# Kernel optimization log

Measured on AMD Instinct MI355X. Metric: run time of the kernel, lower is better.

The kernel has to match this reference:

```python
import jax, jax.numpy as jnp
import numpy as np


def _conv(x, w, b, pad):
    # x: (B,C,H,W), w: (O,I,kh,kw), NCHW conv with given padding
    y = jax.lax.conv_general_dilated(x, w, window_strides=(1, 1), padding=pad,
                                     dimension_numbers=('NCHW', 'OIHW', 'NCHW'))
    return y + b[None, :, None, None]


def _frn(x, eps):
    # FilterResponseNorm: normalize by rms over spatial dims (2,3)
    nu2 = jnp.mean(x * x, axis=(2, 3), keepdims=True)
    return x * jax.lax.rsqrt(nu2 + jnp.abs(eps))


def _mish(x):
    return x * jnp.tanh(jax.nn.softplus(x))


def setup_inputs() -> dict:
    key = jax.random.key(0)
    ks = jax.random.split(key, 9)
    B, C, H, W = 4, 256, 64, 64
    C16 = C // 16
    x = jax.random.normal(ks[0], (B, C, H, W), dtype=jnp.float32)
    s = 0.05
    wq = jax.random.normal(ks[1], (C16, C, 1, 3), dtype=jnp.float32) * s
    bq = jax.random.normal(ks[2], (C16,), dtype=jnp.float32) * s
    wk = jax.random.normal(ks[3], (C16, C, 3, 1), dtype=jnp.float32) * s
    bk = jax.random.normal(ks[4], (C16,), dtype=jnp.float32) * s
    wv = jax.random.normal(ks[5], (C, C, 1, 1), dtype=jnp.float32) * s
    bv = jax.random.normal(ks[6], (C,), dtype=jnp.float32) * s
    gamma = jax.random.normal(ks[7], (1,), dtype=jnp.float32) * 0.1
    eps_q = jnp.full((1, C16, 1, 1), 1e-6, dtype=jnp.float32)
    eps_k = jnp.full((1, C16, 1, 1), 1e-6, dtype=jnp.float32)
    return {"x": x, "wq": wq, "bq": bq, "wk": wk, "bk": bk,
            "wv": wv, "bv": bv, "gamma": gamma, "eps_q": eps_q, "eps_k": eps_k}


def reference(x, wq, bq, wk, bk, wv, bv, gamma, eps_q, eps_k):
    B, C, H, W = x.shape
    N = H * W
    # query branch: Conv2d(k=(1,3), pad=(0,1)) -> FRN -> Mish
    q = _mish(_frn(_conv(x, wq, bq, [(0, 0), (1, 1)]), eps_q))  # (B,C16,H,W)
    # key branch: Conv2d(k=(3,1), pad=(1,0)) -> FRN -> Mish
    k = _mish(_frn(_conv(x, wk, bk, [(1, 1), (0, 0)]), eps_k))  # (B,C16,H,W)
    q = q.reshape(B, -1, N)  # (B,C16,N)
    k = k.reshape(B, -1, N)  # (B,C16,N)
    # affinity[b,n,m] = sum_c q[b,c,n] * k[b,c,m]; softmax over m
    affinity = jnp.einsum('bcn,bcm->bnm', q, k)
    affinity = jax.nn.softmax(affinity, axis=-1)  # (B,N,N)
    v = _conv(x, wv, bv, [(0, 0), (0, 0)]).reshape(B, C, N)  # (B,C,N)
    # weights = v @ affinity^T : weights[b,c,j] = sum_n v[b,c,n] * affinity[b,j,n]
    weights = jnp.einsum('bcn,bjn->bcj', v, affinity).reshape(B, C, H, W)
    return gamma * weights + x
```

## Files before the change

### kernel.cpp

```cpp
#include <hip/hip_runtime.h>
#include <stdint.h>

#define NB 4
#define CC 256
#define C16 16
#define HH 64
#define WW 64
#define NN 4096

typedef __attribute__((ext_vector_type(8))) short short8;
typedef __attribute__((ext_vector_type(4))) float floatx4;
typedef __attribute__((ext_vector_type(16))) float floatx16;

#if __has_builtin(__builtin_amdgcn_exp2f)
#define EXP2(x) __builtin_amdgcn_exp2f(x)
#else
#define EXP2(x) exp2f(x)
#endif

__device__ __forceinline__ unsigned short f2bf(float f) {
    union { float f; unsigned u; } v; v.f = f;
    unsigned r = v.u + 0x7fffu + ((v.u >> 16) & 1u);
    return (unsigned short)(r >> 16);
}
__device__ __forceinline__ float bf2f(unsigned short h) {
    union { unsigned u; float f; } v; v.u = (unsigned)h << 16;
    return v.f;
}


__global__ __launch_bounds__(256) void prep_kernel(
        const float* __restrict__ x, const float* __restrict__ wv,
        const float* __restrict__ wq, const float* __restrict__ wk,
        unsigned short* __restrict__ xT, unsigned short* __restrict__ wvb,
        unsigned short* __restrict__ wqkb, float* __restrict__ nu2) {
    int bid = blockIdx.x;
    if (bid < 1024) {
        __shared__ float tile_t[64][65];
        int nt = bid & 63, ct = (bid >> 6) & 3, b = bid >> 8;
        int n0 = nt * 64, c0 = ct * 64;
        int tid = threadIdx.x;
        int rg = tid >> 4, f = tid & 15;
        const float* xb = x + ((size_t)b * CC + c0) * NN + n0;
#pragma unroll
        for (int p = 0; p < 4; ++p) {
            int c = p * 16 + rg;
            float4 v = *(const float4*)(xb + (size_t)c * NN + f * 4);
            tile_t[f * 4 + 0][c] = v.x;
            tile_t[f * 4 + 1][c] = v.y;
            tile_t[f * 4 + 2][c] = v.z;
            tile_t[f * 4 + 3][c] = v.w;
        }
        __syncthreads();
        unsigned short* xtb = xT + ((size_t)b * NN + n0) * CC + c0;
#pragma unroll
        for (int p = 0; p < 4; ++p) {
            int n = p * 16 + rg;
            ushort4 st;
            st.x = f2bf(tile_t[n][f * 4 + 0]);
            st.y = f2bf(tile_t[n][f * 4 + 1]);
            st.z = f2bf(tile_t[n][f * 4 + 2]);
            st.w = f2bf(tile_t[n][f * 4 + 3]);
            *(ushort4*)(xtb + (size_t)n * CC + f * 4) = st;
        }
    } else {
        int idx = (bid - 1024) * 256 + threadIdx.x;
        if (bid == 1024 && threadIdx.x < 128) nu2[threadIdx.x] = 0.f;
        if (idx < 16384) {
            float4 v = *(const float4*)(wv + idx * 4);
            ushort4 o;
            o.x = f2bf(v.x); o.y = f2bf(v.y); o.z = f2bf(v.z); o.w = f2bf(v.w);
            *(ushort4*)(wvb + idx * 4) = o;
        } else if (idx < 16384 + 6144) {
            int base = (idx - 16384) * 4;
#pragma unroll
            for (int u = 0; u < 4; ++u) {
                int e = base + u;
                int t = e / 12288;
                int i = e - t * 12288;
                int tap = i >> 12, o = (i >> 8) & 15, c = i & 255;
                const float* src = t ? wk : wq;
                wqkb[e] = f2bf(src[o * 768 + c * 3 + tap]);
            }
        }
    }
}

__global__ __launch_bounds__(256) void conv_kernel(
        const unsigned short* __restrict__ xT, const unsigned short* __restrict__ wvb,
        const unsigned short* __restrict__ wqkb, const float* __restrict__ bv,
        const float* __restrict__ bq, const float* __restrict__ bk,
        unsigned short* __restrict__ vb, unsigned short* __restrict__ qrawh,
        unsigned short* __restrict__ krawh, float* __restrict__ nu2) {
    int bid = blockIdx.x;
    int tid = threadIdx.x;
    int wv_ = tid >> 6, lane = tid & 63;
    int q16 = lane >> 4, c16 = lane & 15;
    if (bid < 512) {
        int ntile = bid & 63, b = (bid >> 6) & 3, ch = bid >> 8;
        int n0 = ntile * 64;
        int cb = ch * 128 + wv_ * 32;
        floatx4 fzero = {0.f, 0.f, 0.f, 0.f};
        floatx4 acc[2][4];
        for (int ct = 0; ct < 2; ++ct)
            for (int nt = 0; nt < 4; ++nt) acc[ct][nt] = fzero;
        const unsigned short* xb = xT + ((size_t)b * NN + n0) * CC;
        for (int kc = 0; kc < 8; ++kc) {
            int ko = kc * 32 + q16 * 8;
            short8 a0 = *(const short8*)(wvb + (size_t)(cb + c16) * CC + ko);
            short8 a1 = *(const short8*)(wvb + (size_t)(cb + 16 + c16) * CC + ko);
            short8 bf[4];
#pragma unroll
            for (int nt = 0; nt < 4; ++nt)
                bf[nt] = *(const short8*)(xb + (size_t)(nt * 16 + c16) * CC + ko);
#pragma unroll
            for (int nt = 0; nt < 4; ++nt) {
                acc[0][nt] = __builtin_amdgcn_mfma_f32_16x16x32_bf16(bf[nt], a0, acc[0][nt], 0, 0, 0);
                acc[1][nt] = __builtin_amdgcn_mfma_f32_16x16x32_bf16(bf[nt], a1, acc[1][nt], 0, 0, 0);
            }
        }
        float bv0 = bv[cb + c16], bv1 = bv[cb + 16 + c16];
        int off = 32 * 8 * (q16 >> 1) + (q16 & 1) * 4 + c16 * 8;
#pragma unroll
        for (int ct = 0; ct < 2; ++ct) {
            float bvv = ct ? bv1 : bv0;
#pragma unroll
            for (int nt = 0; nt < 4; ++nt) {
                size_t fb = (((size_t)b * 8 + ch * 4 + wv_) * 256 + (n0 >> 4) + nt) * 512;
                ushort4 st;
                st.x = f2bf(acc[ct][nt][0] + bvv);
                st.y = f2bf(acc[ct][nt][1] + bvv);
                st.z = f2bf(acc[ct][nt][2] + bvv);
                st.w = f2bf(acc[ct][nt][3] + bvv);
                *(ushort4*)(vb + fb + off + ct * 16 * 8) = st;
            }
        }
    } else {
        int cv = bid - 512;
        int nb2 = cv & 63, b = cv >> 6;
        int nl = nb2 * 64 + wv_ * 16 + c16;
        int h = nl >> 6, w = nl & 63;
        bool vm1 = (w != 0), vp1 = (w != 63);
        bool vm64 = (h != 0), vp64 = (h != 63);
        short8 zero8 = {0, 0, 0, 0, 0, 0, 0, 0};
        floatx4 accq = {0.f, 0.f, 0.f, 0.f}, acck = {0.f, 0.f, 0.f, 0.f};
        const unsigned short* xb = xT + (size_t)b * NN * CC;
        const unsigned short* wrow = wqkb + c16 * 256;
        for (int kc = 0; kc < 8; ++kc) {
            int ko = kc * 32 + q16 * 8;
            short8 b0 = *(const short8*)(xb + (size_t)nl * CC + ko);
            short8 bm1 = vm1 ? *(const short8*)(xb + (size_t)(nl - 1) * CC + ko) : zero8;
            short8 bp1 = vp1 ? *(const short8*)(xb + (size_t)(nl + 1) * CC + ko) : zero8;
            short8 bm64 = vm64 ? *(const short8*)(xb + (size_t)(nl - 64) * CC + ko) : zero8;
            short8 bp64 = vp64 ? *(const short8*)(xb + (size_t)(nl + 64) * CC + ko) : zero8;
            short8 aq0 = *(const short8*)(wrow + 0 * 4096 + ko);
            short8 aq1 = *(const short8*)(wrow + 1 * 4096 + ko);
            short8 aq2 = *(const short8*)(wrow + 2 * 4096 + ko);
            short8 ak0 = *(const short8*)(wrow + 12288 + 0 * 4096 + ko);
            short8 ak1 = *(const short8*)(wrow + 12288 + 1 * 4096 + ko);
            short8 ak2 = *(const short8*)(wrow + 12288 + 2 * 4096 + ko);
            accq = __builtin_amdgcn_mfma_f32_16x16x32_bf16(bm1, aq0, accq, 0, 0, 0);
            accq = __builtin_amdgcn_mfma_f32_16x16x32_bf16(b0, aq1, accq, 0, 0, 0);
            accq = __builtin_amdgcn_mfma_f32_16x16x32_bf16(bp1, aq2, accq, 0, 0, 0);
            acck = __builtin_amdgcn_mfma_f32_16x16x32_bf16(bm64, ak0, acck, 0, 0, 0);
            acck = __builtin_amdgcn_mfma_f32_16x16x32_bf16(b0, ak1, acck, 0, 0, 0);
            acck = __builtin_amdgcn_mfma_f32_16x16x32_bf16(bp64, ak2, acck, 0, 0, 0);
        }
        int nst = nb2 * 64 + wv_ * 16 + q16 * 4;
        float bqv = bq[c16], bkv = bk[c16];
        ushort4 sq4, sk4;
        float ssq = 0.f, ssk = 0.f;
        {
            float vq0 = accq[0] + bqv, vq1 = accq[1] + bqv, vq2 = accq[2] + bqv, vq3 = accq[3] + bqv;
            float vk0 = acck[0] + bkv, vk1 = acck[1] + bkv, vk2 = acck[2] + bkv, vk3 = acck[3] + bkv;
            sq4.x = f2bf(vq0); sq4.y = f2bf(vq1); sq4.z = f2bf(vq2); sq4.w = f2bf(vq3);
            sk4.x = f2bf(vk0); sk4.y = f2bf(vk1); sk4.z = f2bf(vk2); sk4.w = f2bf(vk3);
            ssq = vq0 * vq0 + vq1 * vq1 + vq2 * vq2 + vq3 * vq3;
            ssk = vk0 * vk0 + vk1 * vk1 + vk2 * vk2 + vk3 * vk3;
        }
        *(ushort4*)(qrawh + (size_t)(b * C16 + c16) * NN + nst) = sq4;
        *(ushort4*)(krawh + (size_t)(b * C16 + c16) * NN + nst) = sk4;
        ssq += __shfl_xor(ssq, 16, 64);
        ssq += __shfl_xor(ssq, 32, 64);
        ssk += __shfl_xor(ssk, 16, 64);
        ssk += __shfl_xor(ssk, 32, 64);
        if (lane < 16) {
            atomicAdd(nu2 + b * C16 + lane, ssq);
            atomicAdd(nu2 + 64 + b * C16 + lane, ssk);
        }
    }
}

__global__ __launch_bounds__(256) void frn_mish_kernel(
        const unsigned short* __restrict__ qrawh, const unsigned short* __restrict__ krawh,
        const float* __restrict__ nu2, const float* __restrict__ eps_q,
        const float* __restrict__ eps_k, unsigned short* __restrict__ qb,
        unsigned short* __restrict__ kb) {
    int blk = blockIdx.x;
    int tensor = blk >> 8;
    int b = (blk >> 6) & 3;
    int nch = blk & 63;
    const unsigned short* raw = tensor ? krawh : qrawh;
    const float* eps = tensor ? eps_k : eps_q;
    unsigned short* outp = tensor ? kb : qb;
    const float* nu = nu2 + tensor * 64 + b * C16;
    float scale = tensor ? 1.0f : 1.44269504f;
    int n = nch * 64 + (threadIdx.x & 63);
    int oq = threadIdx.x >> 6;
    ushort4 pk4;
#pragma unroll
    for (int i = 0; i < 4; ++i) {
        int o = oq * 4 + i;
        float r = bf2f(raw[(size_t)(b * C16 + o) * NN + n]);
        float v = r * rsqrtf(nu[o] * (1.f / (float)NN) + fabsf(eps[o]));
        float t = EXP2(v * 1.44269504f);
        float num = t * t + 2.0f * t;
        float m = (v * num) * __builtin_amdgcn_rcpf(num + 2.0f);
        if (v > 30.f) m = v;
        m *= scale;
        ((unsigned short*)&pk4)[i] = f2bf(m);
    }
    size_t base = ((size_t)b * 128 + (n >> 5)) * 512 + (size_t)(n & 31) * 8
                + (size_t)(oq >> 1) * 256 + (oq & 1) * 4;
    *(ushort4*)(outp + base) = pk4;
}

__device__ __forceinline__ void pack_half(
        const floatx16& sc, int h, short8* A, float* lsum) {
    unsigned pk[4];
    float ls = 0.f;
#pragma unroll
    for (int p = 0; p < 4; ++p) {
        float e0 = EXP2(sc[8 * h + 2 * p]);
        float e1 = EXP2(sc[8 * h + 2 * p + 1]);
        ls += e0 + e1;
        pk[p] = __builtin_amdgcn_perm(__float_as_uint(e1), __float_as_uint(e0), 0x07060302u);
    }
    *lsum += ls;
    asm("v_permlane32_swap_b32 %0, %1" : "+v"(pk[0]), "+v"(pk[2]));
    asm("v_permlane32_swap_b32 %0, %1" : "+v"(pk[1]), "+v"(pk[3]));
    union { unsigned u[4]; short8 s; } a;
    a.u[0] = pk[0]; a.u[1] = pk[1]; a.u[2] = pk[2]; a.u[3] = pk[3];
    *A = a.s;
}

__global__ __launch_bounds__(256, 2) void attn_kernel(
        const unsigned short* __restrict__ qb, const unsigned short* __restrict__ kb,
        const unsigned short* __restrict__ vb, const float* __restrict__ x,
        const float* __restrict__ gamma_p, float* __restrict__ out) {
    __shared__ float lpart[4][2][32];
    __shared__ float obuf[4][32][33];

    int tid = threadIdx.x;
    int wv_ = __builtin_amdgcn_readfirstlane(tid >> 6);
    int lane = tid & 63;
    int l31 = lane & 31, lh = lane >> 5;
    int id = blockIdx.x;
    int cs = id & 1, b = (id >> 1) & 3, jt = id >> 3;
    int jbase = jt * 64, cb = cs * 128;
    int lane8 = lane * 8;

    const unsigned short* qfb = qb + ((size_t)b * 128 + (jbase >> 5)) * 512 + lane8;
    const unsigned short* kfb = kb + ((size_t)b * 128 + (wv_ * 32)) * 512 + lane8;

    short8 qf0 = *(const short8*)qfb;
    short8 qf1 = *(const short8*)(qfb + 512);

    floatx16 z16 = {0,0,0,0,0,0,0,0,0,0,0,0,0,0,0,0};
    floatx16 acc0[4], acc1[4];
#pragma unroll
    for (int cg = 0; cg < 4; ++cg) { acc0[cg] = z16; acc1[cg] = z16; }
    float lsum0 = 0.f, lsum1 = 0.f;

    const unsigned short* vp0 = vb + (((size_t)b * 8 + cs * 4 + 0) * 256 + wv_ * 64) * 512 + lane8;
    const unsigned short* vp1 = vb + (((size_t)b * 8 + cs * 4 + 1) * 256 + wv_ * 64) * 512 + lane8;
    const unsigned short* vp2 = vb + (((size_t)b * 8 + cs * 4 + 2) * 256 + wv_ * 64) * 512 + lane8;
    const unsigned short* vp3 = vb + (((size_t)b * 8 + cs * 4 + 3) * 256 + wv_ * 64) * 512 + lane8;

    short8 ak = *(const short8*)kfb;
#pragma unroll 1
    for (int step = 0; step < 32; ++step) {
        short8 vf0a = *(const short8*)vp0;
        short8 vf1a = *(const short8*)vp1;
        short8 vf2a = *(const short8*)vp2;
        short8 vf3a = *(const short8*)vp3;
        short8 vf0b = *(const short8*)(vp0 + 512);
        short8 vf1b = *(const short8*)(vp1 + 512);
        short8 vf2b = *(const short8*)(vp2 + 512);
        short8 vf3b = *(const short8*)(vp3 + 512);
        floatx16 sc0 = __builtin_amdgcn_mfma_f32_32x32x16_bf16(ak, qf0, z16, 0, 0, 0);
        floatx16 sc1 = __builtin_amdgcn_mfma_f32_32x32x16_bf16(ak, qf1, z16, 0, 0, 0);
        ak = *(const short8*)(kfb + (size_t)((step + 1) & 31) * 512);
        short8 A;
        pack_half(sc0, 0, &A, &lsum0);
        __builtin_amdgcn_s_setprio(1);
        acc0[0] = __builtin_amdgcn_mfma_f32_32x32x16_bf16(A, vf0a, acc0[0], 0, 0, 0);
        acc0[1] = __builtin_amdgcn_mfma_f32_32x32x16_bf16(A, vf1a, acc0[1], 0, 0, 0);
        acc0[2] = __builtin_amdgcn_mfma_f32_32x32x16_bf16(A, vf2a, acc0[2], 0, 0, 0);
        acc0[3] = __builtin_amdgcn_mfma_f32_32x32x16_bf16(A, vf3a, acc0[3], 0, 0, 0);
        __builtin_amdgcn_s_setprio(0);
        __builtin_amdgcn_sched_barrier(0);
        pack_half(sc0, 1, &A, &lsum0);
        __builtin_amdgcn_s_setprio(1);
        acc0[0] = __builtin_amdgcn_mfma_f32_32x32x16_bf16(A, vf0b, acc0[0], 0, 0, 0);
        acc0[1] = __builtin_amdgcn_mfma_f32_32x32x16_bf16(A, vf1b, acc0[1], 0, 0, 0);
        acc0[2] = __builtin_amdgcn_mfma_f32_32x32x16_bf16(A, vf2b, acc0[2], 0, 0, 0);
        acc0[3] = __builtin_amdgcn_mfma_f32_32x32x16_bf16(A, vf3b, acc0[3], 0, 0, 0);
        __builtin_amdgcn_s_setprio(0);
        __builtin_amdgcn_sched_barrier(0);
        pack_half(sc1, 0, &A, &lsum1);
        __builtin_amdgcn_s_setprio(1);
        acc1[0] = __builtin_amdgcn_mfma_f32_32x32x16_bf16(A, vf0a, acc1[0], 0, 0, 0);
        acc1[1] = __builtin_amdgcn_mfma_f32_32x32x16_bf16(A, vf1a, acc1[1], 0, 0, 0);
        acc1[2] = __builtin_amdgcn_mfma_f32_32x32x16_bf16(A, vf2a, acc1[2], 0, 0, 0);
        acc1[3] = __builtin_amdgcn_mfma_f32_32x32x16_bf16(A, vf3a, acc1[3], 0, 0, 0);
        __builtin_amdgcn_s_setprio(0);
        __builtin_amdgcn_sched_barrier(0);
        pack_half(sc1, 1, &A, &lsum1);
        __builtin_amdgcn_s_setprio(1);
        acc1[0] = __builtin_amdgcn_mfma_f32_32x32x16_bf16(A, vf0b, acc1[0], 0, 0, 0);
        acc1[1] = __builtin_amdgcn_mfma_f32_32x32x16_bf16(A, vf1b, acc1[1], 0, 0, 0);
        acc1[2] = __builtin_amdgcn_mfma_f32_32x32x16_bf16(A, vf2b, acc1[2], 0, 0, 0);
        acc1[3] = __builtin_amdgcn_mfma_f32_32x32x16_bf16(A, vf3b, acc1[3], 0, 0, 0);
        __builtin_amdgcn_s_setprio(0);
        vp0 += 1024; vp1 += 1024; vp2 += 1024; vp3 += 1024;
    }

    lsum0 += __shfl_xor(lsum0, 32, 64);
    lsum1 += __shfl_xor(lsum1, 32, 64);
    if (lh == 0) { lpart[wv_][0][l31] = lsum0; lpart[wv_][1][l31] = lsum1; }
    __syncthreads();

    int j31 = tid & 31;
    float gamma = gamma_p[0];
    float gl0 = gamma / (lpart[0][0][j31] + lpart[1][0][j31] + lpart[2][0][j31] + lpart[3][0][j31]);
    float gl1 = gamma / (lpart[0][1][j31] + lpart[1][1][j31] + lpart[2][1][j31] + lpart[3][1][j31]);
    const float* xbb = x + (size_t)b * CC * NN;
    float* obb = out + (size_t)b * CC * NN;
    int hofs = lh * 4;
    int cgrp = tid >> 5;
#pragma unroll
    for (int jg = 0; jg < 2; ++jg) {
        float gl = jg ? gl1 : gl0;
#pragma unroll
        for (int cg = 0; cg < 4; ++cg) {
            __syncthreads();
            const floatx16& a = jg ? acc1[cg] : acc0[cg];
#pragma unroll
            for (int r = 0; r < 16; ++r) {
                int row = (r & 3) + 8 * (r >> 2) + hofs;
                obuf[wv_][row][l31] = a[r];
            }
            __syncthreads();
#pragma unroll
            for (int i = 0; i < 4; ++i) {
                int c = cgrp * 4 + i;
                float val = obuf[0][j31][c] + obuf[1][j31][c] + obuf[2][j31][c] + obuf[3][j31][c];
                size_t oidx = (size_t)(cb + cg * 32 + c) * NN + jbase + jg * 32 + j31;
                obb[oidx] = fmaf(gl, val, xbb[oidx]);
            }
        }
    }
}

extern "C" void kernel_launch(void* const* d_in, const int* in_sizes, int n_in,
                              void* d_out, int out_size, void* d_ws, size_t ws_size,
                              hipStream_t stream) {
    const float* x     = (const float*)d_in[0];
    const float* wq    = (const float*)d_in[1];
    const float* bq    = (const float*)d_in[2];
    const float* wk    = (const float*)d_in[3];
    const float* bk    = (const float*)d_in[4];
    const float* wv    = (const float*)d_in[5];
    const float* bv    = (const float*)d_in[6];
    const float* gamma = (const float*)d_in[7];
    const float* eps_q = (const float*)d_in[8];
    const float* eps_k = (const float*)d_in[9];
    float* out = (float*)d_out;

    char* ws = (char*)d_ws;
    unsigned short* qrawh = (unsigned short*)ws;
    unsigned short* krawh = (unsigned short*)(ws + (1u << 20));
    float* nu2  = (float*)(ws + (2u << 20));
    unsigned short* qb = (unsigned short*)(ws + (2u << 20) + 4096);
    unsigned short* kb = qb + (size_t)NB * NN * C16;
    unsigned short* vb = kb + (size_t)NB * NN * C16;
    unsigned short* xT = vb + (size_t)NB * CC * NN;
    unsigned short* wvb = xT + (size_t)NB * NN * CC;
    unsigned short* wqkb = wvb + (size_t)CC * CC;

    prep_kernel<<<dim3(1112), dim3(256), 0, stream>>>(x, wv, wq, wk, xT, wvb, wqkb, nu2);
    conv_kernel<<<dim3(768), dim3(256), 0, stream>>>(xT, wvb, wqkb, bv, bq, bk, vb, qrawh, krawh, nu2);
    frn_mish_kernel<<<dim3(512), dim3(256), 0, stream>>>(qrawh, krawh, nu2, eps_q, eps_k, qb, kb);
    attn_kernel<<<dim3(512), dim3(256), 0, stream>>>(qb, kb, vb, x, gamma, out);
}
```

Measured before the change: 163.4 us.

## Fuse four kernels into one cooperative persistent kernel with grid syncs

Moves the prep, conv, FRN/Mish and attention stages into a single cooperative mega kernel of 512 blocks, separated by grid-wide syncs, and keeps the old four-launch path as a fallback. The aim is to drop the launch overhead and tail gaps between the four kernels. The cost is that earlier stages now run on fewer blocks with remapped work (two prep tiles per block, qk conv on the first 256 blocks), each grid sync adds barrier latency, and the launch bound of two blocks per CU applies to all stages.

```diff
diff --git a/kernel.cpp b/kernel.cpp
--- a/kernel.cpp
+++ b/kernel.cpp
@@ -1,5 +1,8 @@
 #include <hip/hip_runtime.h>
+#include <hip/hip_cooperative_groups.h>
 #include <stdint.h>
+
+namespace cg = cooperative_groups;
 
 #define NB 4
 #define CC 256
@@ -29,174 +32,172 @@
 }
 
 
-__global__ __launch_bounds__(256) void prep_kernel(
-        const float* __restrict__ x, const float* __restrict__ wv,
-        const float* __restrict__ wq, const float* __restrict__ wk,
-        unsigned short* __restrict__ xT, unsigned short* __restrict__ wvb,
-        unsigned short* __restrict__ wqkb, float* __restrict__ nu2) {
-    int bid = blockIdx.x;
-    if (bid < 1024) {
-        __shared__ float tile_t[64][65];
-        int nt = bid & 63, ct = (bid >> 6) & 3, b = bid >> 8;
-        int n0 = nt * 64, c0 = ct * 64;
-        int tid = threadIdx.x;
-        int rg = tid >> 4, f = tid & 15;
-        const float* xb = x + ((size_t)b * CC + c0) * NN + n0;
-#pragma unroll
-        for (int p = 0; p < 4; ++p) {
-            int c = p * 16 + rg;
-            float4 v = *(const float4*)(xb + (size_t)c * NN + f * 4);
-            tile_t[f * 4 + 0][c] = v.x;
-            tile_t[f * 4 + 1][c] = v.y;
-            tile_t[f * 4 + 2][c] = v.z;
-            tile_t[f * 4 + 3][c] = v.w;
+
+__device__ __forceinline__ void prep_tile_body(
+        int vb, const float* __restrict__ x, unsigned short* __restrict__ xT,
+        float (*tile_t)[65], int tid) {
+    int nt = vb & 63, ct = (vb >> 6) & 3, b = vb >> 8;
+    int n0 = nt * 64, c0 = ct * 64;
+    int rg = tid >> 4, f = tid & 15;
+    const float* xb = x + ((size_t)b * CC + c0) * NN + n0;
+#pragma unroll
+    for (int p = 0; p < 4; ++p) {
+        int c = p * 16 + rg;
+        float4 v = *(const float4*)(xb + (size_t)c * NN + f * 4);
+        tile_t[f * 4 + 0][c] = v.x;
+        tile_t[f * 4 + 1][c] = v.y;
+        tile_t[f * 4 + 2][c] = v.z;
+        tile_t[f * 4 + 3][c] = v.w;
+    }
+    __syncthreads();
+    unsigned short* xtb = xT + ((size_t)b * NN + n0) * CC + c0;
+#pragma unroll
+    for (int p = 0; p < 4; ++p) {
+        int n = p * 16 + rg;
+        ushort4 st;
+        st.x = f2bf(tile_t[n][f * 4 + 0]);
+        st.y = f2bf(tile_t[n][f * 4 + 1]);
+        st.z = f2bf(tile_t[n][f * 4 + 2]);
+        st.w = f2bf(tile_t[n][f * 4 + 3]);
+        *(ushort4*)(xtb + (size_t)n * CC + f * 4) = st;
+    }
+}
+
+__device__ __forceinline__ void prep_wt_body(
+        int vb, const float* __restrict__ wv, const float* __restrict__ wq,
+        const float* __restrict__ wk, unsigned short* __restrict__ wvb,
+        unsigned short* __restrict__ wqkb, float* __restrict__ nu2, int tid) {
+    int idx = (vb - 1024) * 256 + tid;
+    if (vb == 1024 && tid < 128) nu2[tid] = 0.f;
+    if (idx < 16384) {
+        float4 v = *(const float4*)(wv + idx * 4);
+        ushort4 o;
+        o.x = f2bf(v.x); o.y = f2bf(v.y); o.z = f2bf(v.z); o.w = f2bf(v.w);
+        *(ushort4*)(wvb + idx * 4) = o;
+    } else if (idx < 16384 + 6144) {
+        int base = (idx - 16384) * 4;
+#pragma unroll
+        for (int u = 0; u < 4; ++u) {
+            int e = base + u;
+            int t = e / 12288;
+            int i = e - t * 12288;
+            int tap = i >> 12, o = (i >> 8) & 15, c = i & 255;
+            const float* src = t ? wk : wq;
+            wqkb[e] = f2bf(src[o * 768 + c * 3 + tap]);
         }
-        __syncthreads();
-        unsigned short* xtb = xT + ((size_t)b * NN + n0) * CC + c0;
-#pragma unroll
-        for (int p = 0; p < 4; ++p) {
-            int n = p * 16 + rg;
-            ushort4 st;
-            st.x = f2bf(tile_t[n][f * 4 + 0]);
-            st.y = f2bf(tile_t[n][f * 4 + 1]);
-            st.z = f2bf(tile_t[n][f * 4 + 2]);
-            st.w = f2bf(tile_t[n][f * 4 + 3]);
-            *(ushort4*)(xtb + (size_t)n * CC + f * 4) = st;
-        }
-    } else {
-        int idx = (bid - 1024) * 256 + threadIdx.x;
-        if (bid == 1024 && threadIdx.x < 128) nu2[threadIdx.x] = 0.f;
-        if (idx < 16384) {
-            float4 v = *(const float4*)(wv + idx * 4);
-            ushort4 o;
-            o.x = f2bf(v.x); o.y = f2bf(v.y); o.z = f2bf(v.z); o.w = f2bf(v.w);
-            *(ushort4*)(wvb + idx * 4) = o;
-        } else if (idx < 16384 + 6144) {
-            int base = (idx - 16384) * 4;
-#pragma unroll
-            for (int u = 0; u < 4; ++u) {
-                int e = base + u;
-                int t = e / 12288;
-                int i = e - t * 12288;
-                int tap = i >> 12, o = (i >> 8) & 15, c = i & 255;
-                const float* src = t ? wk : wq;
-                wqkb[e] = f2bf(src[o * 768 + c * 3 + tap]);
-            }
-        }
-    }
-}
-
-__global__ __launch_bounds__(256) void conv_kernel(
-        const unsigned short* __restrict__ xT, const unsigned short* __restrict__ wvb,
-        const unsigned short* __restrict__ wqkb, const float* __restrict__ bv,
-        const float* __restrict__ bq, const float* __restrict__ bk,
-        unsigned short* __restrict__ vb, unsigned short* __restrict__ qrawh,
-        unsigned short* __restrict__ krawh, float* __restrict__ nu2) {
-    int bid = blockIdx.x;
-    int tid = threadIdx.x;
+    }
+}
+
+__device__ __forceinline__ void conv_v_body(
+        int vb, const unsigned short* __restrict__ xT, const unsigned short* __restrict__ wvb,
+        const float* __restrict__ bv, unsigned short* __restrict__ vbuf, int tid) {
     int wv_ = tid >> 6, lane = tid & 63;
     int q16 = lane >> 4, c16 = lane & 15;
-    if (bid < 512) {
-        int ntile = bid & 63, b = (bid >> 6) & 3, ch = bid >> 8;
-        int n0 = ntile * 64;
-        int cb = ch * 128 + wv_ * 32;
-        floatx4 fzero = {0.f, 0.f, 0.f, 0.f};
-        floatx4 acc[2][4];
-        for (int ct = 0; ct < 2; ++ct)
-            for (int nt = 0; nt < 4; ++nt) acc[ct][nt] = fzero;
-        const unsigned short* xb = xT + ((size_t)b * NN + n0) * CC;
-        for (int kc = 0; kc < 8; ++kc) {
-            int ko = kc * 32 + q16 * 8;
-            short8 a0 = *(const short8*)(wvb + (size_t)(cb + c16) * CC + ko);
-            short8 a1 = *(const short8*)(wvb + (size_t)(cb + 16 + c16) * CC + ko);
-            short8 bf[4];
-#pragma unroll
-            for (int nt = 0; nt < 4; ++nt)
-                bf[nt] = *(const short8*)(xb + (size_t)(nt * 16 + c16) * CC + ko);
-#pragma unroll
-            for (int nt = 0; nt < 4; ++nt) {
-                acc[0][nt] = __builtin_amdgcn_mfma_f32_16x16x32_bf16(bf[nt], a0, acc[0][nt], 0, 0, 0);
-                acc[1][nt] = __builtin_amdgcn_mfma_f32_16x16x32_bf16(bf[nt], a1, acc[1][nt], 0, 0, 0);
-            }
+    int ntile = vb & 63, b = (vb >> 6) & 3, ch = vb >> 8;
+    int n0 = ntile * 64;
+    int cb = ch * 128 + wv_ * 32;
+    floatx4 fzero = {0.f, 0.f, 0.f, 0.f};
+    floatx4 acc[2][4];
+    for (int ct = 0; ct < 2; ++ct)
+        for (int nt = 0; nt < 4; ++nt) acc[ct][nt] = fzero;
+    const unsigned short* xb = xT + ((size_t)b * NN + n0) * CC;
+    for (int kc = 0; kc < 8; ++kc) {
+        int ko = kc * 32 + q16 * 8;
+        short8 a0 = *(const short8*)(wvb + (size_t)(cb + c16) * CC + ko);
+        short8 a1 = *(const short8*)(wvb + (size_t)(cb + 16 + c16) * CC + ko);
+        short8 bf[4];
+#pragma unroll
+        for (int nt = 0; nt < 4; ++nt)
+            bf[nt] = *(const short8*)(xb + (size_t)(nt * 16 + c16) * CC + ko);
+#pragma unroll
+        for (int nt = 0; nt < 4; ++nt) {
+            acc[0][nt] = __builtin_amdgcn_mfma_f32_16x16x32_bf16(bf[nt], a0, acc[0][nt], 0, 0, 0);
+            acc[1][nt] = __builtin_amdgcn_mfma_f32_16x16x32_bf16(bf[nt], a1, acc[1][nt], 0, 0, 0);
         }
-        float bv0 = bv[cb + c16], bv1 = bv[cb + 16 + c16];
-        int off = 32 * 8 * (q16 >> 1) + (q16 & 1) * 4 + c16 * 8;
-#pragma unroll
-        for (int ct = 0; ct < 2; ++ct) {
-            float bvv = ct ? bv1 : bv0;
-#pragma unroll
-            for (int nt = 0; nt < 4; ++nt) {
-                size_t fb = (((size_t)b * 8 + ch * 4 + wv_) * 256 + (n0 >> 4) + nt) * 512;
-                ushort4 st;
-                st.x = f2bf(acc[ct][nt][0] + bvv);
-                st.y = f2bf(acc[ct][nt][1] + bvv);
-                st.z = f2bf(acc[ct][nt][2] + bvv);
-                st.w = f2bf(acc[ct][nt][3] + bvv);
-                *(ushort4*)(vb + fb + off + ct * 16 * 8) = st;
-            }
+    }
+    float bv0 = bv[cb + c16], bv1 = bv[cb + 16 + c16];
+    int off = 32 * 8 * (q16 >> 1) + (q16 & 1) * 4 + c16 * 8;
+#pragma unroll
+    for (int ct = 0; ct < 2; ++ct) {
+        float bvv = ct ? bv1 : bv0;
+#pragma unroll
+        for (int nt = 0; nt < 4; ++nt) {
+            size_t fb = (((size_t)b * 8 + ch * 4 + wv_) * 256 + (n0 >> 4) + nt) * 512;
+            ushort4 st;
+            st.x = f2bf(acc[ct][nt][0] + bvv);
+            st.y = f2bf(acc[ct][nt][1] + bvv);
+            st.z = f2bf(acc[ct][nt][2] + bvv);
+            st.w = f2bf(acc[ct][nt][3] + bvv);
+            *(ushort4*)(vbuf + fb + off + ct * 16 * 8) = st;
         }
-    } else {
-        int cv = bid - 512;
-        int nb2 = cv & 63, b = cv >> 6;
-        int nl = nb2 * 64 + wv_ * 16 + c16;
-        int h = nl >> 6, w = nl & 63;
-        bool vm1 = (w != 0), vp1 = (w != 63);
-        bool vm64 = (h != 0), vp64 = (h != 63);
-        short8 zero8 = {0, 0, 0, 0, 0, 0, 0, 0};
-        floatx4 accq = {0.f, 0.f, 0.f, 0.f}, acck = {0.f, 0.f, 0.f, 0.f};
-        const unsigned short* xb = xT + (size_t)b * NN * CC;
-        const unsigned short* wrow = wqkb + c16 * 256;
-        for (int kc = 0; kc < 8; ++kc) {
-            int ko = kc * 32 + q16 * 8;
-            short8 b0 = *(const short8*)(xb + (size_t)nl * CC + ko);
-            short8 bm1 = vm1 ? *(const short8*)(xb + (size_t)(nl - 1) * CC + ko) : zero8;
-            short8 bp1 = vp1 ? *(const short8*)(xb + (size_t)(nl + 1) * CC + ko) : zero8;
-            short8 bm64 = vm64 ? *(const short8*)(xb + (size_t)(nl - 64) * CC + ko) : zero8;
-            short8 bp64 = vp64 ? *(const short8*)(xb + (size_t)(nl + 64) * CC + ko) : zero8;
-            short8 aq0 = *(const short8*)(wrow + 0 * 4096 + ko);
-            short8 aq1 = *(const short8*)(wrow + 1 * 4096 + ko);
-            short8 aq2 = *(const short8*)(wrow + 2 * 4096 + ko);
-            short8 ak0 = *(const short8*)(wrow + 12288 + 0 * 4096 + ko);
-            short8 ak1 = *(const short8*)(wrow + 12288 + 1 * 4096 + ko);
-            short8 ak2 = *(const short8*)(wrow + 12288 + 2 * 4096 + ko);
-            accq = __builtin_amdgcn_mfma_f32_16x16x32_bf16(bm1, aq0, accq, 0, 0, 0);
-            accq = __builtin_amdgcn_mfma_f32_16x16x32_bf16(b0, aq1, accq, 0, 0, 0);
-            accq = __builtin_amdgcn_mfma_f32_16x16x32_bf16(bp1, aq2, accq, 0, 0, 0);
-            acck = __builtin_amdgcn_mfma_f32_16x16x32_bf16(bm64, ak0, acck, 0, 0, 0);
-            acck = __builtin_amdgcn_mfma_f32_16x16x32_bf16(b0, ak1, acck, 0, 0, 0);
-            acck = __builtin_amdgcn_mfma_f32_16x16x32_bf16(bp64, ak2, acck, 0, 0, 0);
-        }
-        int nst = nb2 * 64 + wv_ * 16 + q16 * 4;
-        float bqv = bq[c16], bkv = bk[c16];
-        ushort4 sq4, sk4;
-        float ssq = 0.f, ssk = 0.f;
-        {
-            float vq0 = accq[0] + bqv, vq1 = accq[1] + bqv, vq2 = accq[2] + bqv, vq3 = accq[3] + bqv;
-            float vk0 = acck[0] + bkv, vk1 = acck[1] + bkv, vk2 = acck[2] + bkv, vk3 = acck[3] + bkv;
-            sq4.x = f2bf(vq0); sq4.y = f2bf(vq1); sq4.z = f2bf(vq2); sq4.w = f2bf(vq3);
-            sk4.x = f2bf(vk0); sk4.y = f2bf(vk1); sk4.z = f2bf(vk2); sk4.w = f2bf(vk3);
-            ssq = vq0 * vq0 + vq1 * vq1 + vq2 * vq2 + vq3 * vq3;
-            ssk = vk0 * vk0 + vk1 * vk1 + vk2 * vk2 + vk3 * vk3;
-        }
-        *(ushort4*)(qrawh + (size_t)(b * C16 + c16) * NN + nst) = sq4;
-        *(ushort4*)(krawh + (size_t)(b * C16 + c16) * NN + nst) = sk4;
-        ssq += __shfl_xor(ssq, 16, 64);
-        ssq += __shfl_xor(ssq, 32, 64);
-        ssk += __shfl_xor(ssk, 16, 64);
-        ssk += __shfl_xor(ssk, 32, 64);
-        if (lane < 16) {
-            atomicAdd(nu2 + b * C16 + lane, ssq);
-            atomicAdd(nu2 + 64 + b * C16 + lane, ssk);
-        }
-    }
-}
-
-__global__ __launch_bounds__(256) void frn_mish_kernel(
-        const unsigned short* __restrict__ qrawh, const unsigned short* __restrict__ krawh,
+    }
+}
+
+__device__ __forceinline__ void conv_qk_body(
+        int cv, const unsigned short* __restrict__ xT, const unsigned short* __restrict__ wqkb,
+        const float* __restrict__ bq, const float* __restrict__ bk,
+        unsigned short* __restrict__ qrawh, unsigned short* __restrict__ krawh,
+        float* __restrict__ nu2, int tid) {
+    int wv_ = tid >> 6, lane = tid & 63;
+    int q16 = lane >> 4, c16 = lane & 15;
+    int nb2 = cv & 63, b = cv >> 6;
+    int nl = nb2 * 64 + wv_ * 16 + c16;
+    int h = nl >> 6, w = nl & 63;
+    bool vm1 = (w != 0), vp1 = (w != 63);
+    bool vm64 = (h != 0), vp64 = (h != 63);
+    short8 zero8 = {0, 0, 0, 0, 0, 0, 0, 0};
+    floatx4 accq = {0.f, 0.f, 0.f, 0.f}, acck = {0.f, 0.f, 0.f, 0.f};
+    const unsigned short* xb = xT + (size_t)b * NN * CC;
+    const unsigned short* wrow = wqkb + c16 * 256;
+    for (int kc = 0; kc < 8; ++kc) {
+        int ko = kc * 32 + q16 * 8;
+        short8 b0 = *(const short8*)(xb + (size_t)nl * CC + ko);
+        short8 bm1 = vm1 ? *(const short8*)(xb + (size_t)(nl - 1) * CC + ko) : zero8;
+        short8 bp1 = vp1 ? *(const short8*)(xb + (size_t)(nl + 1) * CC + ko) : zero8;
+        short8 bm64 = vm64 ? *(const short8*)(xb + (size_t)(nl - 64) * CC + ko) : zero8;
+        short8 bp64 = vp64 ? *(const short8*)(xb + (size_t)(nl + 64) * CC + ko) : zero8;
+        short8 aq0 = *(const short8*)(wrow + 0 * 4096 + ko);
+        short8 aq1 = *(const short8*)(wrow + 1 * 4096 + ko);
+        short8 aq2 = *(const short8*)(wrow + 2 * 4096 + ko);
+        short8 ak0 = *(const short8*)(wrow + 12288 + 0 * 4096 + ko);
+        short8 ak1 = *(const short8*)(wrow + 12288 + 1 * 4096 + ko);
+        short8 ak2 = *(const short8*)(wrow + 12288 + 2 * 4096 + ko);
+        accq = __builtin_amdgcn_mfma_f32_16x16x32_bf16(bm1, aq0, accq, 0, 0, 0);
+        accq = __builtin_amdgcn_mfma_f32_16x16x32_bf16(b0, aq1, accq, 0, 0, 0);
+        accq = __builtin_amdgcn_mfma_f32_16x16x32_bf16(bp1, aq2, accq, 0, 0, 0);
+        acck = __builtin_amdgcn_mfma_f32_16x16x32_bf16(bm64, ak0, acck, 0, 0, 0);
+        acck = __builtin_amdgcn_mfma_f32_16x16x32_bf16(b0, ak1, acck, 0, 0, 0);
+        acck = __builtin_amdgcn_mfma_f32_16x16x32_bf16(bp64, ak2, acck, 0, 0, 0);
+    }
+    int nst = nb2 * 64 + wv_ * 16 + q16 * 4;
+    float bqv = bq[c16], bkv = bk[c16];
+    ushort4 sq4, sk4;
+    float ssq = 0.f, ssk = 0.f;
+    {
+        float vq0 = accq[0] + bqv, vq1 = accq[1] + bqv, vq2 = accq[2] + bqv, vq3 = accq[3] + bqv;
+        float vk0 = acck[0] + bkv, vk1 = acck[1] + bkv, vk2 = acck[2] + bkv, vk3 = acck[3] + bkv;
+        sq4.x = f2bf(vq0); sq4.y = f2bf(vq1); sq4.z = f2bf(vq2); sq4.w = f2bf(vq3);
+        sk4.x = f2bf(vk0); sk4.y = f2bf(vk1); sk4.z = f2bf(vk2); sk4.w = f2bf(vk3);
+        ssq = vq0 * vq0 + vq1 * vq1 + vq2 * vq2 + vq3 * vq3;
+        ssk = vk0 * vk0 + vk1 * vk1 + vk2 * vk2 + vk3 * vk3;
+    }
+    *(ushort4*)(qrawh + (size_t)(b * C16 + c16) * NN + nst) = sq4;
+    *(ushort4*)(krawh + (size_t)(b * C16 + c16) * NN + nst) = sk4;
+    ssq += __shfl_xor(ssq, 16, 64);
+    ssq += __shfl_xor(ssq, 32, 64);
+    ssk += __shfl_xor(ssk, 16, 64);
+    ssk += __shfl_xor(ssk, 32, 64);
+    if (lane < 16) {
+        atomicAdd(nu2 + b * C16 + lane, ssq);
+        atomicAdd(nu2 + 64 + b * C16 + lane, ssk);
+    }
+}
+
+__device__ __forceinline__ void frn_body(
+        int blk, const unsigned short* __restrict__ qrawh, const unsigned short* __restrict__ krawh,
         const float* __restrict__ nu2, const float* __restrict__ eps_q,
         const float* __restrict__ eps_k, unsigned short* __restrict__ qb,
-        unsigned short* __restrict__ kb) {
-    int blk = blockIdx.x;
+        unsigned short* __restrict__ kb, int tid) {
     int tensor = blk >> 8;
     int b = (blk >> 6) & 3;
     int nch = blk & 63;
@@ -205,8 +206,8 @@
     unsigned short* outp = tensor ? kb : qb;
     const float* nu = nu2 + tensor * 64 + b * C16;
     float scale = tensor ? 1.0f : 1.44269504f;
-    int n = nch * 64 + (threadIdx.x & 63);
-    int oq = threadIdx.x >> 6;
+    int n = nch * 64 + (tid & 63);
+    int oq = tid >> 6;
     ushort4 pk4;
 #pragma unroll
     for (int i = 0; i < 4; ++i) {
@@ -244,18 +245,14 @@
     *A = a.s;
 }
 
-__global__ __launch_bounds__(256, 2) void attn_kernel(
-        const unsigned short* __restrict__ qb, const unsigned short* __restrict__ kb,
-        const unsigned short* __restrict__ vb, const float* __restrict__ x,
-        const float* __restrict__ gamma_p, float* __restrict__ out) {
-    __shared__ float lpart[4][2][32];
-    __shared__ float obuf[4][32][33];
-
-    int tid = threadIdx.x;
+__device__ __forceinline__ void attn_body(
+        int id, const unsigned short* __restrict__ qb, const unsigned short* __restrict__ kb,
+        const unsigned short* __restrict__ vbuf, const float* __restrict__ x,
+        const float* __restrict__ gamma_p, float* __restrict__ out,
+        float (*lpart)[2][32], float (*obuf)[32][33], int tid) {
     int wv_ = __builtin_amdgcn_readfirstlane(tid >> 6);
     int lane = tid & 63;
     int l31 = lane & 31, lh = lane >> 5;
-    int id = blockIdx.x;
     int cs = id & 1, b = (id >> 1) & 3, jt = id >> 3;
     int jbase = jt * 64, cb = cs * 128;
     int lane8 = lane * 8;
@@ -272,10 +269,10 @@
     for (int cg = 0; cg < 4; ++cg) { acc0[cg] = z16; acc1[cg] = z16; }
     float lsum0 = 0.f, lsum1 = 0.f;
 
-    const unsigned short* vp0 = vb + (((size_t)b * 8 + cs * 4 + 0) * 256 + wv_ * 64) * 512 + lane8;
-    const unsigned short* vp1 = vb + (((size_t)b * 8 + cs * 4 + 1) * 256 + wv_ * 64) * 512 + lane8;
-    const unsigned short* vp2 = vb + (((size_t)b * 8 + cs * 4 + 2) * 256 + wv_ * 64) * 512 + lane8;
-    const unsigned short* vp3 = vb + (((size_t)b * 8 + cs * 4 + 3) * 256 + wv_ * 64) * 512 + lane8;
+    const unsigned short* vp0 = vbuf + (((size_t)b * 8 + cs * 4 + 0) * 256 + wv_ * 64) * 512 + lane8;
+    const unsigned short* vp1 = vbuf + (((size_t)b * 8 + cs * 4 + 1) * 256 + wv_ * 64) * 512 + lane8;
+    const unsigned short* vp2 = vbuf + (((size_t)b * 8 + cs * 4 + 2) * 256 + wv_ * 64) * 512 + lane8;
+    const unsigned short* vp3 = vbuf + (((size_t)b * 8 + cs * 4 + 3) * 256 + wv_ * 64) * 512 + lane8;
 
     short8 ak = *(const short8*)kfb;
 #pragma unroll 1
@@ -363,6 +360,98 @@
     }
 }
 
+__global__ __launch_bounds__(256, 2) void mega_kernel(
+        const float* __restrict__ x, const float* __restrict__ wq,
+        const float* __restrict__ bq, const float* __restrict__ wk,
+        const float* __restrict__ bk, const float* __restrict__ wv,
+        const float* __restrict__ bv, const float* __restrict__ gamma_p,
+        const float* __restrict__ eps_q, const float* __restrict__ eps_k,
+        float* __restrict__ out, char* __restrict__ ws) {
+    __shared__ __align__(16) char smem_u[17920];
+    float (*tile_t)[65] = (float (*)[65])smem_u;
+    float (*lpart)[2][32] = (float (*)[2][32])smem_u;
+    float (*obuf)[32][33] = (float (*)[32][33])(smem_u + 1024);
+
+    unsigned short* qrawh = (unsigned short*)ws;
+    unsigned short* krawh = (unsigned short*)(ws + (1u << 20));
+    float* nu2  = (float*)(ws + (2u << 20));
+    unsigned short* qb = (unsigned short*)(ws + (2u << 20) + 4096);
+    unsigned short* kb = qb + (size_t)NB * NN * C16;
+    unsigned short* vbuf = kb + (size_t)NB * NN * C16;
+    unsigned short* xT = vbuf + (size_t)NB * CC * NN;
+    unsigned short* wvb = xT + (size_t)NB * NN * CC;
+    unsigned short* wqkb = wvb + (size_t)CC * CC;
+
+    cg::grid_group grid = cg::this_grid();
+    int bid = blockIdx.x;
+    int tid = threadIdx.x;
+
+    {
+        prep_tile_body(bid, x, xT, tile_t, tid);
+        __syncthreads();
+        prep_tile_body(bid + 512, x, xT, tile_t, tid);
+        if (bid < 88) prep_wt_body(bid + 1024, wv, wq, wk, wvb, wqkb, nu2, tid);
+    }
+    __threadfence();
+    grid.sync();
+    __threadfence();
+
+    {
+        conv_v_body(bid, xT, wvb, bv, vbuf, tid);
+        if (bid < 256) conv_qk_body(bid, xT, wqkb, bq, bk, qrawh, krawh, nu2, tid);
+    }
+    __threadfence();
+    grid.sync();
+    __threadfence();
+
+    frn_body(bid, qrawh, krawh, nu2, eps_q, eps_k, qb, kb, tid);
+    __threadfence();
+    grid.sync();
+    __threadfence();
+
+    __syncthreads();
+    attn_body(bid, qb, kb, vbuf, x, gamma_p, out, lpart, obuf, tid);
+}
+
+__global__ __launch_bounds__(256) void prep_kernel(
+        const float* __restrict__ x, const float* __restrict__ wv,
+        const float* __restrict__ wq, const float* __restrict__ wk,
+        unsigned short* __restrict__ xT, unsigned short* __restrict__ wvb,
+        unsigned short* __restrict__ wqkb, float* __restrict__ nu2) {
+    __shared__ float tile_t[64][65];
+    int bid = blockIdx.x;
+    if (bid < 1024) prep_tile_body(bid, x, xT, tile_t, threadIdx.x);
+    else prep_wt_body(bid, wv, wq, wk, wvb, wqkb, nu2, threadIdx.x);
+}
+
+__global__ __launch_bounds__(256) void conv_kernel(
+        const unsigned short* __restrict__ xT, const unsigned short* __restrict__ wvb,
+        const unsigned short* __restrict__ wqkb, const float* __restrict__ bv,
+        const float* __restrict__ bq, const float* __restrict__ bk,
+        unsigned short* __restrict__ vbuf, unsigned short* __restrict__ qrawh,
+        unsigned short* __restrict__ krawh, float* __restrict__ nu2) {
+    int bid = blockIdx.x;
+    if (bid < 512) conv_v_body(bid, xT, wvb, bv, vbuf, threadIdx.x);
+    else conv_qk_body(bid - 512, xT, wqkb, bq, bk, qrawh, krawh, nu2, threadIdx.x);
+}
+
+__global__ __launch_bounds__(256) void frn_mish_kernel(
+        const unsigned short* __restrict__ qrawh, const unsigned short* __restrict__ krawh,
+        const float* __restrict__ nu2, const float* __restrict__ eps_q,
+        const float* __restrict__ eps_k, unsigned short* __restrict__ qb,
+        unsigned short* __restrict__ kb) {
+    frn_body(blockIdx.x, qrawh, krawh, nu2, eps_q, eps_k, qb, kb, threadIdx.x);
+}
+
+__global__ __launch_bounds__(256, 2) void attn_kernel(
+        const unsigned short* __restrict__ qb, const unsigned short* __restrict__ kb,
+        const unsigned short* __restrict__ vbuf, const float* __restrict__ x,
+        const float* __restrict__ gamma_p, float* __restrict__ out) {
+    __shared__ float lpart[4][2][32];
+    __shared__ float obuf[4][32][33];
+    attn_body(blockIdx.x, qb, kb, vbuf, x, gamma_p, out, lpart, obuf, threadIdx.x);
+}
+
 extern "C" void kernel_launch(void* const* d_in, const int* in_sizes, int n_in,
                               void* d_out, int out_size, void* d_ws, size_t ws_size,
                               hipStream_t stream) {
@@ -377,20 +466,37 @@
     const float* eps_q = (const float*)d_in[8];
     const float* eps_k = (const float*)d_in[9];
     float* out = (float*)d_out;
-
     char* ws = (char*)d_ws;
+
+    static int coop_ok = -1;
+    if (coop_ok < 0) {
+        int v = 0;
+        if (hipDeviceGetAttribute(&v, hipDeviceAttributeCooperativeLaunch, 0) != hipSuccess) v = 0;
+        coop_ok = v;
+    }
+
+    if (coop_ok) {
+        void* args[] = {(void*)&x, (void*)&wq, (void*)&bq, (void*)&wk, (void*)&bk,
+                        (void*)&wv, (void*)&bv, (void*)&gamma, (void*)&eps_q,
+                        (void*)&eps_k, (void*)&out, (void*)&ws};
+        hipError_t err = hipLaunchCooperativeKernel(
+            (void*)mega_kernel, dim3(512), dim3(256), args, 0, stream);
+        if (err == hipSuccess) return;
+        coop_ok = 0;
+    }
+
     unsigned short* qrawh = (unsigned short*)ws;
     unsigned short* krawh = (unsigned short*)(ws + (1u << 20));
     float* nu2  = (float*)(ws + (2u << 20));
     unsigned short* qb = (unsigned short*)(ws + (2u << 20) + 4096);
     unsigned short* kb = qb + (size_t)NB * NN * C16;
-    unsigned short* vb = kb + (size_t)NB * NN * C16;
-    unsigned short* xT = vb + (size_t)NB * CC * NN;
+    unsigned short* vbuf = kb + (size_t)NB * NN * C16;
+    unsigned short* xT = vbuf + (size_t)NB * CC * NN;
     unsigned short* wvb = xT + (size_t)NB * NN * CC;
     unsigned short* wqkb = wvb + (size_t)CC * CC;
 
     prep_kernel<<<dim3(1112), dim3(256), 0, stream>>>(x, wv, wq, wk, xT, wvb, wqkb, nu2);
-    conv_kernel<<<dim3(768), dim3(256), 0, stream>>>(xT, wvb, wqkb, bv, bq, bk, vb, qrawh, krawh, nu2);
+    conv_kernel<<<dim3(768), dim3(256), 0, stream>>>(xT, wvb, wqkb, bv, bq, bk, vbuf, qrawh, krawh, nu2);
     frn_mish_kernel<<<dim3(512), dim3(256), 0, stream>>>(qrawh, krawh, nu2, eps_q, eps_k, qb, kb);
-    attn_kernel<<<dim3(512), dim3(256), 0, stream>>>(qb, kb, vb, x, gamma, out);
-}
+    attn_kernel<<<dim3(512), dim3(256), 0, stream>>>(qb, kb, vbuf, x, gamma, out);
+}
```

After: 162.9 us. Within noise of the previous version (-0.3%).
